# Optimization experiments

Hardware: AMD Instinct MI355X
Metric: run time of the kernel (lower is better)

Reference implementation:

```python
import jax, jax.numpy as jnp
import numpy as np

N_NODES = 160000
N_EDGES = 2560000
N_GRAPHS = 1024
D = 32


def _gcn_layer(x, W, b, row, col, w):
    # PyG GCNConv with add_self_loops=True (loop weight 1) and symmetric norm.
    xw = x @ W                                   # [N, D]
    deg = jax.ops.segment_sum(w, col, num_segments=N_NODES) + 1.0  # self-loop
    dinv = jax.lax.rsqrt(deg)                    # deg >= 1 so finite
    norm = dinv[row] * w * dinv[col]             # [E]
    agg = jax.ops.segment_sum(norm[:, None] * xw[row], col, num_segments=N_NODES)
    agg = agg + xw * (1.0 / deg)[:, None]        # self-loop message: dinv[i]^2 = 1/deg[i]
    return agg + b


def setup_inputs() -> dict:
    key = jax.random.key(0)
    ks = jax.random.split(key, 20)
    s = 0.1
    inp = {
        "x": jax.random.normal(ks[0], (N_NODES, 1), jnp.float32),
        "edge_indices": jax.random.randint(ks[1], (2, N_EDGES), 0, N_NODES),
        "edge_weights": jax.random.uniform(ks[2], (N_EDGES,), jnp.float32),
        "batch": jnp.sort(jax.random.randint(ks[3], (N_NODES,), 0, N_GRAPHS)),
        # pre-MLP (2 layers)
        "W_pre0": s * jax.random.normal(ks[4], (1, D), jnp.float32),
        "b_pre0": jnp.zeros((D,), jnp.float32),
        "W_pre1": s * jax.random.normal(ks[5], (D, D), jnp.float32),
        "b_pre1": jnp.zeros((D,), jnp.float32),
        # 3 GCNConv layers
        "W_g0": s * jax.random.normal(ks[6], (D, D), jnp.float32),
        "b_g0": jnp.zeros((D,), jnp.float32),
        "W_g1": s * jax.random.normal(ks[7], (D, D), jnp.float32),
        "b_g1": jnp.zeros((D,), jnp.float32),
        "W_g2": s * jax.random.normal(ks[8], (D, D), jnp.float32),
        "b_g2": jnp.zeros((D,), jnp.float32),
        # post-MLP (2 layers, last -> 1 + sigmoid)
        "W_post0": s * jax.random.normal(ks[9], (D, D), jnp.float32),
        "b_post0": jnp.zeros((D,), jnp.float32),
        "W_post1": s * jax.random.normal(ks[10], (D, 1), jnp.float32),
        "b_post1": jnp.zeros((1,), jnp.float32),
    }
    return inp


def reference(x, edge_indices, edge_weights, batch,
              W_pre0, b_pre0, W_pre1, b_pre1,
              W_g0, b_g0, W_g1, b_g1, W_g2, b_g2,
              W_post0, b_post0, W_post1, b_post1):
    row, col = edge_indices[0], edge_indices[1]
    # pre-MLP: Linear + ReLU x2
    h = jax.nn.relu(x @ W_pre0 + b_pre0)
    h = jax.nn.relu(h @ W_pre1 + b_pre1)
    h = jax.nn.relu(_gcn_layer(h, W_g0, b_g0, row, col, edge_weights))
    h = jax.nn.relu(_gcn_layer(h, W_g1, b_g1, row, col, edge_weights))
    h = jax.nn.relu(_gcn_layer(h, W_g2, b_g2, row, col, edge_weights))
    # global mean pool over batch ids
    sums = jax.ops.segment_sum(h, batch, num_segments=N_GRAPHS)
    cnts = jax.ops.segment_sum(jnp.ones((N_NODES,), h.dtype), batch, num_segments=N_GRAPHS)
    g = sums / jnp.maximum(cnts, 1.0)[:, None]
    # post-MLP: Linear+ReLU (dropout inactive in eval), then Linear+Sigmoid
    g = jax.nn.relu(g @ W_post0 + b_post0)
    out = jax.nn.sigmoid(g @ W_post1 + b_post1)
    return out
```

## Files before the change

### kernel.cpp

```cpp
#include <hip/hip_runtime.h>
#include <math.h>

#define DIM 32
#define NB 625
#define CAP 5120
#define CHUNK 8192
#define BMAX 7424

typedef float floatx2 __attribute__((ext_vector_type(2)));

__device__ __forceinline__ unsigned pack4_fp8(float a, float b, float c, float d) {
    unsigned v = 0;
    v = __builtin_amdgcn_cvt_pk_fp8_f32(a, b, v, false);
    v = __builtin_amdgcn_cvt_pk_fp8_f32(c, d, v, true);
    return v;
}

__global__ void setup_kernel(const int* __restrict__ batch, int* __restrict__ gptr,
                             int* __restrict__ bcur, int N, int G) {
    int n = blockIdx.x * blockDim.x + threadIdx.x;
    if (n < NB) bcur[n] = n * CAP;
    if (n >= N) return;
    int b = batch[n];
    int bp = (n == 0) ? -1 : batch[n - 1];
    for (int g = bp + 1; g <= b; g++) gptr[g] = n;
    if (n == N - 1) {
        for (int g = b + 1; g <= G; g++) gptr[g] = N;
    }
}

__global__ __launch_bounds__(1024) void passA_kernel(
        const int* __restrict__ row, const int* __restrict__ col,
        const float* __restrict__ w, int* __restrict__ bcur,
        unsigned long long* __restrict__ stage, int E) {
    __shared__ unsigned long long lrec[CHUNK];
    __shared__ int hist[NB];
    __shared__ int excl[NB + 1];
    __shared__ int gbase[NB];
    __shared__ int sc[1024];
    int t = threadIdx.x;
    int base = blockIdx.x * CHUNK;
    int cnt = min(CHUNK, E - base);
    int creg[8];

    for (int j = t; j < NB; j += 1024) hist[j] = 0;
    __syncthreads();

#pragma unroll
    for (int i = 0; i < 8; i++) {
        int e = base + i * 1024 + t;
        creg[i] = (e < E) ? col[e] : -1;
        if (creg[i] >= 0) atomicAdd(&hist[creg[i] >> 8], 1);
    }
    __syncthreads();

    int v = (t < NB) ? hist[t] : 0;
    sc[t] = v;
    __syncthreads();
#pragma unroll
    for (int off = 1; off < 1024; off <<= 1) {
        int u = (t >= off) ? sc[t - off] : 0;
        __syncthreads();
        sc[t] += u;
        __syncthreads();
    }
    if (t < NB) {
        int ex = sc[t] - v;
        excl[t] = ex;
        hist[t] = ex;
        gbase[t] = v ? atomicAdd(&bcur[t], v) : 0;
    }
    if (t == 0) excl[NB] = cnt;
    __syncthreads();

#pragma unroll
    for (int i = 0; i < 8; i++) {
        int e = base + i * 1024 + t;
        int c = creg[i];
        if (c >= 0) {
            unsigned long long rec = ((unsigned long long)(unsigned)row[e] << 40)
                                   | ((unsigned long long)(unsigned)(c & 255) << 32)
                                   | (unsigned long long)__float_as_uint(w[e]);
            int pos = atomicAdd(&hist[c >> 8], 1);
            lrec[pos] = rec;
        }
    }
    __syncthreads();

    for (int i = t; i < cnt; i += 1024) {
        int lo = 0, hi = NB;
        while (hi - lo > 1) {
            int mid = (lo + hi) >> 1;
            if (excl[mid] <= i) lo = mid; else hi = mid;
        }
        int gpos = gbase[lo] + (i - excl[lo]);
        if (gpos < (lo + 1) * CAP) stage[gpos] = lrec[i];
    }
}

__global__ void passB1_kernel(const unsigned long long* __restrict__ stage,
                              const int* __restrict__ bcur,
                              int* __restrict__ cnt, float* __restrict__ dinv) {
    __shared__ int icnt[256];
    __shared__ float fdeg[256];
    int b = blockIdx.x;
    icnt[threadIdx.x] = 0;
    fdeg[threadIdx.x] = 0.0f;
    __syncthreads();
    int s0 = b * CAP;
    int m = min(bcur[b] - s0, CAP);
    for (int i = threadIdx.x; i < m; i += 256) {
        unsigned long long rec = stage[s0 + i];
        int cj = (int)((rec >> 32) & 255);
        float wf = __uint_as_float((unsigned)rec);
        atomicAdd(&icnt[cj], 1);
        atomicAdd(&fdeg[cj], wf);
    }
    __syncthreads();
    int c = b * 256 + threadIdx.x;
    cnt[c] = ((icnt[threadIdx.x] + 8) >> 3) << 3;
    dinv[c] = rsqrtf(fdeg[threadIdx.x] + 1.0f);
}

__global__ void scan_block_kernel(const int* __restrict__ cnt, int* __restrict__ ptr,
                                  int* __restrict__ bsum, int N) {
    __shared__ int s[256];
    int i = blockIdx.x * 256 + threadIdx.x;
    int v = (i < N) ? cnt[i] : 0;
    s[threadIdx.x] = v;
    __syncthreads();
#pragma unroll
    for (int off = 1; off < 256; off <<= 1) {
        int t = (threadIdx.x >= off) ? s[threadIdx.x - off] : 0;
        __syncthreads();
        s[threadIdx.x] += t;
        __syncthreads();
    }
    if (i < N) ptr[i] = s[threadIdx.x] - v;
    if (threadIdx.x == 255) bsum[blockIdx.x] = s[255];
}

__global__ void scan_fin_kernel(int* __restrict__ ptr, const int* __restrict__ bsum,
                                int N) {
    __shared__ int red[256];
    int b = blockIdx.x;
    int t = threadIdx.x;
    int p = 0;
    for (int j = t; j < b; j += 256) p += bsum[j];
    red[t] = p;
    __syncthreads();
#pragma unroll
    for (int off = 128; off > 0; off >>= 1) {
        if (t < off) red[t] += red[t + off];
        __syncthreads();
    }
    int S = red[0];
    int i = b * 256 + t;
    if (i < N) ptr[i] += S;
    if (b == gridDim.x - 1 && t == 0) ptr[N] = S + bsum[b];
}

__global__ void passB2_kernel(const unsigned long long* __restrict__ stage,
                              const int* __restrict__ bcur, const int* __restrict__ ptr,
                              const float* __restrict__ dinv,
                              unsigned* __restrict__ edat) {
    __shared__ unsigned limg[BMAX];
    __shared__ int lcur[256];
    __shared__ int s_pbase, s_pend;
    int b = blockIdx.x;
    int t = threadIdx.x;
    int c = b * 256 + t;
    int p0 = ptr[c];
    if (t == 0) s_pbase = p0;
    if (t == 255) s_pend = ptr[c + 1];
    __syncthreads();
    int pbase = s_pbase;
    int sz = s_pend - pbase;
    lcur[t] = p0 - pbase + 1;
    for (int i = t; i < sz; i += 256) limg[i] = 0;
    __syncthreads();
    float di = dinv[c];
    float d2 = di * di;
    unsigned qs = min((unsigned)(d2 * 16384.0f + 0.5f), 16383u);
    limg[p0 - pbase] = ((unsigned)c << 14) | qs;
    int s0 = b * CAP;
    int m = min(bcur[b] - s0, CAP);
    for (int i = t; i < m; i += 256) {
        unsigned long long rec = stage[s0 + i];
        int r = (int)(rec >> 40);
        int cj = (int)((rec >> 32) & 255);
        float wf = __uint_as_float((unsigned)rec);
        float nm = dinv[r] * wf * dinv[b * 256 + cj];
        unsigned q = (unsigned)(nm * 16384.0f + 0.5f);
        q = min(q, 16383u);
        int pos = atomicAdd(&lcur[cj], 1);
        limg[pos] = ((unsigned)r << 14) | q;
    }
    __syncthreads();
    for (int i = t; i < sz; i += 256) edat[pbase + i] = limg[i];
}

__global__ void pre_kernel(const float* __restrict__ x,
                           const float* __restrict__ W0, const float* __restrict__ b0,
                           const float* __restrict__ W1, const float* __restrict__ b1,
                           const float* __restrict__ Wg,
                           unsigned char* __restrict__ xw8, int N) {
    int n = blockIdx.x * blockDim.x + threadIdx.x;
    if (n >= N) return;
    float xv = x[n];
    float h0[DIM];
#pragma unroll
    for (int k = 0; k < DIM; k++) h0[k] = fmaxf(xv * W0[k] + b0[k], 0.0f);
    float h1[DIM];
#pragma unroll
    for (int d = 0; d < DIM; d++) h1[d] = b1[d];
#pragma unroll
    for (int k = 0; k < DIM; k++) {
        float hk = h0[k];
#pragma unroll
        for (int d = 0; d < DIM; d++) h1[d] += hk * W1[k * DIM + d];
    }
#pragma unroll
    for (int d = 0; d < DIM; d++) h1[d] = fmaxf(h1[d], 0.0f);
    float o[DIM];
#pragma unroll
    for (int d = 0; d < DIM; d++) o[d] = 0.0f;
#pragma unroll
    for (int k = 0; k < DIM; k++) {
        float hk = h1[k];
#pragma unroll
        for (int d = 0; d < DIM; d++) o[d] += hk * Wg[k * DIM + d];
    }
    unsigned u[8];
#pragma unroll
    for (int i = 0; i < 8; i++)
        u[i] = pack4_fp8(o[4 * i], o[4 * i + 1], o[4 * i + 2], o[4 * i + 3]);
    uint4* dst = (uint4*)(xw8 + (size_t)n * 32);
    dst[0] = make_uint4(u[0], u[1], u[2], u[3]);
    dst[1] = make_uint4(u[4], u[5], u[6], u[7]);
}

__device__ __forceinline__ void gather_body(
        const unsigned char* __restrict__ xin, const unsigned* __restrict__ edat,
        int e0, int e1, int slot, int sub, float acc[8]) {
    floatx2 a0 = {0, 0}, a1 = {0, 0}, a2 = {0, 0}, a3 = {0, 0};
    for (int base = e0; base < e1; base += 8) {
        unsigned rec0 = edat[base + slot];
        unsigned rec1 = edat[base + 4 + slot];
        int r0 = (int)(rec0 >> 14);
        int r1 = (int)(rec1 >> 14);
        float nm0 = (float)(rec0 & 16383u) * (1.0f / 16384.0f);
        float nm1 = (float)(rec1 & 16383u) * (1.0f / 16384.0f);
        uint2 u0 = *(const uint2*)(xin + (size_t)r0 * 32 + sub * 8);
        uint2 u1 = *(const uint2*)(xin + (size_t)r1 * 32 + sub * 8);
        floatx2 w0; w0.x = nm0; w0.y = nm0;
        floatx2 w1; w1.x = nm1; w1.y = nm1;
        a0 += w0 * __builtin_amdgcn_cvt_pk_f32_fp8(u0.x, false);
        a1 += w0 * __builtin_amdgcn_cvt_pk_f32_fp8(u0.x, true);
        a2 += w0 * __builtin_amdgcn_cvt_pk_f32_fp8(u0.y, false);
        a3 += w0 * __builtin_amdgcn_cvt_pk_f32_fp8(u0.y, true);
        a0 += w1 * __builtin_amdgcn_cvt_pk_f32_fp8(u1.x, false);
        a1 += w1 * __builtin_amdgcn_cvt_pk_f32_fp8(u1.x, true);
        a2 += w1 * __builtin_amdgcn_cvt_pk_f32_fp8(u1.y, false);
        a3 += w1 * __builtin_amdgcn_cvt_pk_f32_fp8(u1.y, true);
    }
    acc[0] = a0.x; acc[1] = a0.y; acc[2] = a1.x; acc[3] = a1.y;
    acc[4] = a2.x; acc[5] = a2.y; acc[6] = a3.x; acc[7] = a3.y;
#pragma unroll
    for (int s = 8; s >= 4; s >>= 1) {
#pragma unroll
        for (int i = 0; i < 8; i++) acc[i] += __shfl_xor(acc[i], s, 64);
    }
}

__global__ void gm_kernel(const unsigned char* __restrict__ xin,
                          const unsigned* __restrict__ edat,
                          const int* __restrict__ ptr,
                          const float* __restrict__ bgl,
                          const float* __restrict__ Wn,
                          unsigned char* __restrict__ xout, int N) {
    __shared__ float hs[16][33];
    __shared__ float wsm[1024];
    int t = threadIdx.x;
    for (int j = t; j < 1024; j += 256) wsm[j] = Wn[j];
    int wv = (blockIdx.x * blockDim.x + t) >> 6;
    int n0 = wv * 4;
    int lane = t & 63;
    int sg   = lane >> 4;
    int slot = (lane >> 2) & 3;
    int sub  = lane & 3;
    int n = n0 + sg;
    int e0 = ptr[n], e1 = ptr[n + 1];
    float acc[8];
    gather_body(xin, edat, e0, e1, slot, sub, acc);
    if (slot == 0) {
        int ln = (t >> 6) * 4 + sg;
#pragma unroll
        for (int i = 0; i < 8; i++)
            hs[ln][sub * 8 + i] = fmaxf(acc[i] + bgl[sub * 8 + i], 0.0f);
    }
    __syncthreads();
    int ln = t >> 4, dg = t & 15;
    const float* hrow = hs[ln];
    float o0 = 0.0f, o1 = 0.0f;
#pragma unroll
    for (int k = 0; k < DIM; k++) {
        float hk = hrow[k];
        o0 += hk * wsm[k * DIM + dg * 2];
        o1 += hk * wsm[k * DIM + dg * 2 + 1];
    }
    unsigned v = __builtin_amdgcn_cvt_pk_fp8_f32(o0, o1, 0, false);
    int nodeG = blockIdx.x * 16 + ln;
    *(unsigned short*)(xout + (size_t)nodeG * 32 + dg * 2) = (unsigned short)(v & 0xffff);
}

__global__ void gather_kernel(const unsigned char* __restrict__ xw8,
                              const unsigned* __restrict__ edat,
                              const int* __restrict__ ptr,
                              const float* __restrict__ bg,
                              float* __restrict__ agg, int N) {
    int wv = (blockIdx.x * blockDim.x + threadIdx.x) >> 6;
    int n0 = wv * 4;
    if (n0 >= N) return;
    int lane = threadIdx.x & 63;
    int sg   = lane >> 4;
    int slot = (lane >> 2) & 3;
    int sub  = lane & 3;
    int n = n0 + sg;
    int e0 = ptr[n], e1 = ptr[n + 1];
    float acc[8];
    gather_body(xw8, edat, e0, e1, slot, sub, acc);
    if (slot == 0) {
        float4 v0 = make_float4(acc[0] + bg[sub * 8 + 0], acc[1] + bg[sub * 8 + 1],
                                acc[2] + bg[sub * 8 + 2], acc[3] + bg[sub * 8 + 3]);
        float4 v1 = make_float4(acc[4] + bg[sub * 8 + 4], acc[5] + bg[sub * 8 + 5],
                                acc[6] + bg[sub * 8 + 6], acc[7] + bg[sub * 8 + 7]);
        float4* dst = (float4*)(agg + (size_t)n * DIM + sub * 8);
        dst[0] = v0;
        dst[1] = v1;
    }
}

__global__ void pool_post_kernel(const float* __restrict__ agg, const int* __restrict__ gptr,
                                 const float* __restrict__ W0, const float* __restrict__ b0,
                                 const float* __restrict__ W1, const float* __restrict__ b1,
                                 float* __restrict__ out) {
    __shared__ float red[8][DIM];
    __shared__ float gv[DIM];
    __shared__ float pr[DIM];
    int g = blockIdx.x;
    int s0 = gptr[g], s1 = gptr[g + 1];
    int slot = threadIdx.x >> 5, d = threadIdx.x & 31;
    float acc = 0.0f;
    for (int n = s0 + slot; n < s1; n += 8)
        acc += fmaxf(agg[(size_t)n * DIM + d], 0.0f);
    red[slot][d] = acc;
    __syncthreads();
    if (threadIdx.x < DIM) {
        float t = 0.0f;
#pragma unroll
        for (int i = 0; i < 8; i++) t += red[i][threadIdx.x];
        float c = fmaxf((float)(s1 - s0), 1.0f);
        gv[threadIdx.x] = t / c;
    }
    __syncthreads();
    if (threadIdx.x < DIM) {
        int j = threadIdx.x;
        float p = b0[j];
#pragma unroll
        for (int k = 0; k < DIM; k++) p += gv[k] * W0[k * DIM + j];
        pr[j] = fmaxf(p, 0.0f) * W1[j];
    }
    __syncthreads();
    if (threadIdx.x == 0) {
        float a = b1[0];
#pragma unroll
        for (int j = 0; j < DIM; j++) a += pr[j];
        out[g] = 1.0f / (1.0f + expf(-a));
    }
}

extern "C" void kernel_launch(void* const* d_in, const int* in_sizes, int n_in,
                              void* d_out, int out_size, void* d_ws, size_t ws_size,
                              hipStream_t stream) {
    const float* x   = (const float*)d_in[0];
    const int*   ei  = (const int*)d_in[1];
    const float* ew  = (const float*)d_in[2];
    const int*   bat = (const int*)d_in[3];
    const float* Wpre0 = (const float*)d_in[4];
    const float* bpre0 = (const float*)d_in[5];
    const float* Wpre1 = (const float*)d_in[6];
    const float* bpre1 = (const float*)d_in[7];
    const float* Wg[3]  = {(const float*)d_in[8],  (const float*)d_in[10], (const float*)d_in[12]};
    const float* bg[3]  = {(const float*)d_in[9],  (const float*)d_in[11], (const float*)d_in[13]};
    const float* Wpost0 = (const float*)d_in[14];
    const float* bpost0 = (const float*)d_in[15];
    const float* Wpost1 = (const float*)d_in[16];
    const float* bpost1 = (const float*)d_in[17];
    float* out = (float*)d_out;

    const int N = in_sizes[0];
    const int E = in_sizes[2];
    const int G = out_size;
    const int nb = (N + 255) / 256;

    const int* row = ei;
    const int* col = ei + E;

    float* ws = (float*)d_ws;
    size_t nd = (size_t)N * DIM;
    float*          agg   = ws;
    unsigned char*  xw8a  = (unsigned char*)(agg + nd);
    unsigned long long* stage = (unsigned long long*)ws;
    float*          dinv  = ws + nd + nd / 4;
    int*            cnt   = (int*)(dinv + N);
    int*            ptr   = cnt + N;
    int*            bsum  = ptr + (N + 2);
    int*            gptr  = bsum + 626;
    int*            bcur  = gptr + 1026;
    unsigned*       edat  = (unsigned*)(bcur + 626);
    unsigned char*  xw8b  = (unsigned char*)(edat + E + 8 * (size_t)N);

    const int B = 256;

    setup_kernel<<<(N + B - 1) / B, B, 0, stream>>>(bat, gptr, bcur, N, G);
    int nChunksA = (E + CHUNK - 1) / CHUNK;
    passA_kernel<<<nChunksA, 1024, 0, stream>>>(row, col, ew, bcur, stage, E);
    passB1_kernel<<<NB, B, 0, stream>>>(stage, bcur, cnt, dinv);
    scan_block_kernel<<<nb, 256, 0, stream>>>(cnt, ptr, bsum, N);
    scan_fin_kernel<<<nb, 256, 0, stream>>>(ptr, bsum, N);
    passB2_kernel<<<NB, B, 0, stream>>>(stage, bcur, ptr, dinv, edat);

    pre_kernel<<<(N + B - 1) / B, B, 0, stream>>>(
        x, Wpre0, bpre0, Wpre1, bpre1, Wg[0], xw8a, N);

    long long gThreads = (long long)(N / 4) * 64;
    int gBlocks = (int)((gThreads + B - 1) / B);
    int fBlocks = N / 16;

    gm_kernel<<<fBlocks, B, 0, stream>>>(xw8a, edat, ptr, bg[0], Wg[1], xw8b, N);
    gm_kernel<<<fBlocks, B, 0, stream>>>(xw8b, edat, ptr, bg[1], Wg[2], xw8a, N);
    gather_kernel<<<gBlocks, B, 0, stream>>>(xw8a, edat, ptr, bg[2], agg, N);

    pool_post_kernel<<<G, 256, 0, stream>>>(agg, gptr, Wpost0, bpost0, Wpost1, bpost1, out);
}
```

Baseline: 310.1 us.

## Fuse CSR scan into build passes and pool the last layer via atomics

The block-local exclusive scan moves into passB1, and the cross-block offset into passB2, so two separate scan kernels disappear and passB2 writes final CSR pointers itself. The last gather layer now applies bias and ReLU and atomically adds into per-graph sums, with wave-level shuffle reduction when all four nodes belong to one graph. This removes the N×32 float agg round-trip and the pooling kernel's read of it, leaving a small post-MLP kernel. It trades this for float atomics, so the summation order becomes non-deterministic, and for more per-block prefix work in passB2.

```diff
diff --git a/kernel.cpp b/kernel.cpp
--- a/kernel.cpp
+++ b/kernel.cpp
@@ -17,9 +17,11 @@
 }
 
 __global__ void setup_kernel(const int* __restrict__ batch, int* __restrict__ gptr,
-                             int* __restrict__ bcur, int N, int G) {
+                             int* __restrict__ bcur, float* __restrict__ gsum,
+                             int N, int G) {
     int n = blockIdx.x * blockDim.x + threadIdx.x;
     if (n < NB) bcur[n] = n * CAP;
+    if (n < G * DIM) gsum[n] = 0.0f;
     if (n >= N) return;
     int b = batch[n];
     int bp = (n == 0) ? -1 : batch[n - 1];
@@ -100,16 +102,19 @@
 
 __global__ void passB1_kernel(const unsigned long long* __restrict__ stage,
                               const int* __restrict__ bcur,
-                              int* __restrict__ cnt, float* __restrict__ dinv) {
+                              int* __restrict__ ptr, int* __restrict__ bsum,
+                              float* __restrict__ dinv) {
     __shared__ int icnt[256];
     __shared__ float fdeg[256];
+    __shared__ int s[256];
     int b = blockIdx.x;
-    icnt[threadIdx.x] = 0;
-    fdeg[threadIdx.x] = 0.0f;
+    int t = threadIdx.x;
+    icnt[t] = 0;
+    fdeg[t] = 0.0f;
     __syncthreads();
     int s0 = b * CAP;
     int m = min(bcur[b] - s0, CAP);
-    for (int i = threadIdx.x; i < m; i += 256) {
+    for (int i = t; i < m; i += 256) {
         unsigned long long rec = stage[s0 + i];
         int cj = (int)((rec >> 32) & 255);
         float wf = __uint_as_float((unsigned)rec);
@@ -117,34 +122,33 @@
         atomicAdd(&fdeg[cj], wf);
     }
     __syncthreads();
-    int c = b * 256 + threadIdx.x;
-    cnt[c] = ((icnt[threadIdx.x] + 8) >> 3) << 3;
-    dinv[c] = rsqrtf(fdeg[threadIdx.x] + 1.0f);
-}
-
-__global__ void scan_block_kernel(const int* __restrict__ cnt, int* __restrict__ ptr,
-                                  int* __restrict__ bsum, int N) {
-    __shared__ int s[256];
-    int i = blockIdx.x * 256 + threadIdx.x;
-    int v = (i < N) ? cnt[i] : 0;
-    s[threadIdx.x] = v;
+    int c = b * 256 + t;
+    int v = ((icnt[t] + 8) >> 3) << 3;
+    dinv[c] = rsqrtf(fdeg[t] + 1.0f);
+    s[t] = v;
     __syncthreads();
 #pragma unroll
     for (int off = 1; off < 256; off <<= 1) {
-        int t = (threadIdx.x >= off) ? s[threadIdx.x - off] : 0;
+        int u = (t >= off) ? s[t - off] : 0;
         __syncthreads();
-        s[threadIdx.x] += t;
+        s[t] += u;
         __syncthreads();
     }
-    if (i < N) ptr[i] = s[threadIdx.x] - v;
-    if (threadIdx.x == 255) bsum[blockIdx.x] = s[255];
-}
-
-__global__ void scan_fin_kernel(int* __restrict__ ptr, const int* __restrict__ bsum,
-                                int N) {
+    ptr[c] = s[t] - v;
+    if (t == 255) bsum[b] = s[255];
+}
+
+__global__ void passB2_kernel(const unsigned long long* __restrict__ stage,
+                              const int* __restrict__ bcur, int* __restrict__ ptr,
+                              const int* __restrict__ bsum,
+                              const float* __restrict__ dinv,
+                              unsigned* __restrict__ edat, int N) {
+    __shared__ unsigned limg[BMAX];
+    __shared__ int lcur[256];
     __shared__ int red[256];
     int b = blockIdx.x;
     int t = threadIdx.x;
+    int c = b * 256 + t;
     int p = 0;
     for (int j = t; j < b; j += 256) p += bsum[j];
     red[t] = p;
@@ -155,34 +159,15 @@
         __syncthreads();
     }
     int S = red[0];
-    int i = b * 256 + t;
-    if (i < N) ptr[i] += S;
-    if (b == gridDim.x - 1 && t == 0) ptr[N] = S + bsum[b];
-}
-
-__global__ void passB2_kernel(const unsigned long long* __restrict__ stage,
-                              const int* __restrict__ bcur, const int* __restrict__ ptr,
-                              const float* __restrict__ dinv,
-                              unsigned* __restrict__ edat) {
-    __shared__ unsigned limg[BMAX];
-    __shared__ int lcur[256];
-    __shared__ int s_pbase, s_pend;
-    int b = blockIdx.x;
-    int t = threadIdx.x;
-    int c = b * 256 + t;
-    int p0 = ptr[c];
-    if (t == 0) s_pbase = p0;
-    if (t == 255) s_pend = ptr[c + 1];
-    __syncthreads();
-    int pbase = s_pbase;
-    int sz = s_pend - pbase;
-    lcur[t] = p0 - pbase + 1;
-    for (int i = t; i < sz; i += 256) limg[i] = 0;
+    int bs = bsum[b];
+    int pl = ptr[c];
+    lcur[t] = pl + 1;
+    for (int i = t; i < bs; i += 256) limg[i] = 0;
     __syncthreads();
     float di = dinv[c];
     float d2 = di * di;
     unsigned qs = min((unsigned)(d2 * 16384.0f + 0.5f), 16383u);
-    limg[p0 - pbase] = ((unsigned)c << 14) | qs;
+    limg[pl] = ((unsigned)c << 14) | qs;
     int s0 = b * CAP;
     int m = min(bcur[b] - s0, CAP);
     for (int i = t; i < m; i += 256) {
@@ -197,7 +182,9 @@
         limg[pos] = ((unsigned)r << 14) | q;
     }
     __syncthreads();
-    for (int i = t; i < sz; i += 256) edat[pbase + i] = limg[i];
+    for (int i = t; i < bs; i += 256) edat[S + i] = limg[i];
+    ptr[c] = S + pl;
+    if (b == gridDim.x - 1 && t == 255) ptr[N] = S + bs;
 }
 
 __global__ void pre_kernel(const float* __restrict__ x,
@@ -314,11 +301,12 @@
     *(unsigned short*)(xout + (size_t)nodeG * 32 + dg * 2) = (unsigned short)(v & 0xffff);
 }
 
-__global__ void gather_kernel(const unsigned char* __restrict__ xw8,
-                              const unsigned* __restrict__ edat,
-                              const int* __restrict__ ptr,
-                              const float* __restrict__ bg,
-                              float* __restrict__ agg, int N) {
+__global__ void gp_kernel(const unsigned char* __restrict__ xw8,
+                          const unsigned* __restrict__ edat,
+                          const int* __restrict__ ptr,
+                          const int* __restrict__ batch,
+                          const float* __restrict__ bg,
+                          float* __restrict__ gsum, int N) {
     int wv = (blockIdx.x * blockDim.x + threadIdx.x) >> 6;
     int n0 = wv * 4;
     if (n0 >= N) return;
@@ -330,54 +318,50 @@
     int e0 = ptr[n], e1 = ptr[n + 1];
     float acc[8];
     gather_body(xw8, edat, e0, e1, slot, sub, acc);
-    if (slot == 0) {
-        float4 v0 = make_float4(acc[0] + bg[sub * 8 + 0], acc[1] + bg[sub * 8 + 1],
-                                acc[2] + bg[sub * 8 + 2], acc[3] + bg[sub * 8 + 3]);
-        float4 v1 = make_float4(acc[4] + bg[sub * 8 + 4], acc[5] + bg[sub * 8 + 5],
-                                acc[6] + bg[sub * 8 + 6], acc[7] + bg[sub * 8 + 7]);
-        float4* dst = (float4*)(agg + (size_t)n * DIM + sub * 8);
-        dst[0] = v0;
-        dst[1] = v1;
-    }
-}
-
-__global__ void pool_post_kernel(const float* __restrict__ agg, const int* __restrict__ gptr,
-                                 const float* __restrict__ W0, const float* __restrict__ b0,
-                                 const float* __restrict__ W1, const float* __restrict__ b1,
-                                 float* __restrict__ out) {
-    __shared__ float red[8][DIM];
-    __shared__ float gv[DIM];
-    __shared__ float pr[DIM];
-    int g = blockIdx.x;
-    int s0 = gptr[g], s1 = gptr[g + 1];
-    int slot = threadIdx.x >> 5, d = threadIdx.x & 31;
-    float acc = 0.0f;
-    for (int n = s0 + slot; n < s1; n += 8)
-        acc += fmaxf(agg[(size_t)n * DIM + d], 0.0f);
-    red[slot][d] = acc;
-    __syncthreads();
-    if (threadIdx.x < DIM) {
-        float t = 0.0f;
-#pragma unroll
-        for (int i = 0; i < 8; i++) t += red[i][threadIdx.x];
-        float c = fmaxf((float)(s1 - s0), 1.0f);
-        gv[threadIdx.x] = t / c;
-    }
-    __syncthreads();
-    if (threadIdx.x < DIM) {
-        int j = threadIdx.x;
-        float p = b0[j];
-#pragma unroll
-        for (int k = 0; k < DIM; k++) p += gv[k] * W0[k * DIM + j];
-        pr[j] = fmaxf(p, 0.0f) * W1[j];
-    }
-    __syncthreads();
-    if (threadIdx.x == 0) {
-        float a = b1[0];
-#pragma unroll
-        for (int j = 0; j < DIM; j++) a += pr[j];
-        out[g] = 1.0f / (1.0f + expf(-a));
-    }
+    float v[8];
+#pragma unroll
+    for (int i = 0; i < 8; i++) v[i] = fmaxf(acc[i] + bg[sub * 8 + i], 0.0f);
+    int g0 = batch[n0];
+    int g3 = batch[n0 + 3];
+    if (g0 == g3) {
+#pragma unroll
+        for (int i = 0; i < 8; i++) {
+            v[i] += __shfl_xor(v[i], 16, 64);
+            v[i] += __shfl_xor(v[i], 32, 64);
+        }
+        if (lane < 4) {
+#pragma unroll
+            for (int i = 0; i < 8; i++)
+                atomicAdd(&gsum[g0 * DIM + sub * 8 + i], v[i]);
+        }
+    } else {
+        if (slot == 0) {
+            int g = batch[n];
+#pragma unroll
+            for (int i = 0; i < 8; i++)
+                atomicAdd(&gsum[g * DIM + sub * 8 + i], v[i]);
+        }
+    }
+}
+
+__global__ void post_kernel(const float* __restrict__ gsum, const int* __restrict__ gptr,
+                            const float* __restrict__ W0, const float* __restrict__ b0,
+                            const float* __restrict__ W1, const float* __restrict__ b1,
+                            float* __restrict__ out, int G) {
+    __shared__ float gv[8][DIM];
+    int t = threadIdx.x;
+    int li = t & 31, gi = t >> 5;
+    int g = blockIdx.x * 8 + gi;
+    float cnt = fmaxf((float)(gptr[g + 1] - gptr[g]), 1.0f);
+    gv[gi][li] = gsum[g * DIM + li] / cnt;
+    __syncthreads();
+    float p = b0[li];
+#pragma unroll
+    for (int k = 0; k < DIM; k++) p += gv[gi][k] * W0[k * DIM + li];
+    float pj = fmaxf(p, 0.0f) * W1[li];
+#pragma unroll
+    for (int s = 16; s > 0; s >>= 1) pj += __shfl_xor(pj, s, 32);
+    if (li == 0) out[g] = 1.0f / (1.0f + expf(-(pj + b1[0])));
 }
 
 extern "C" void kernel_launch(void* const* d_in, const int* in_sizes, int n_in,
@@ -402,34 +386,30 @@
     const int N = in_sizes[0];
     const int E = in_sizes[2];
     const int G = out_size;
-    const int nb = (N + 255) / 256;
 
     const int* row = ei;
     const int* col = ei + E;
 
     float* ws = (float*)d_ws;
     size_t nd = (size_t)N * DIM;
-    float*          agg   = ws;
-    unsigned char*  xw8a  = (unsigned char*)(agg + nd);
     unsigned long long* stage = (unsigned long long*)ws;
+    unsigned char*  xw8a  = (unsigned char*)(ws + nd);
     float*          dinv  = ws + nd + nd / 4;
-    int*            cnt   = (int*)(dinv + N);
-    int*            ptr   = cnt + N;
+    int*            ptr   = (int*)(dinv + N);
     int*            bsum  = ptr + (N + 2);
     int*            gptr  = bsum + 626;
     int*            bcur  = gptr + 1026;
-    unsigned*       edat  = (unsigned*)(bcur + 626);
+    float*          gsum  = (float*)(bcur + 626);
+    unsigned*       edat  = (unsigned*)(gsum + (size_t)G * DIM);
     unsigned char*  xw8b  = (unsigned char*)(edat + E + 8 * (size_t)N);
 
     const int B = 256;
 
-    setup_kernel<<<(N + B - 1) / B, B, 0, stream>>>(bat, gptr, bcur, N, G);
+    setup_kernel<<<(N + B - 1) / B, B, 0, stream>>>(bat, gptr, bcur, gsum, N, G);
     int nChunksA = (E + CHUNK - 1) / CHUNK;
     passA_kernel<<<nChunksA, 1024, 0, stream>>>(row, col, ew, bcur, stage, E);
-    passB1_kernel<<<NB, B, 0, stream>>>(stage, bcur, cnt, dinv);
-    scan_block_kernel<<<nb, 256, 0, stream>>>(cnt, ptr, bsum, N);
-    scan_fin_kernel<<<nb, 256, 0, stream>>>(ptr, bsum, N);
-    passB2_kernel<<<NB, B, 0, stream>>>(stage, bcur, ptr, dinv, edat);
+    passB1_kernel<<<NB, B, 0, stream>>>(stage, bcur, ptr, bsum, dinv);
+    passB2_kernel<<<NB, B, 0, stream>>>(stage, bcur, ptr, bsum, dinv, edat, N);
 
     pre_kernel<<<(N + B - 1) / B, B, 0, stream>>>(
         x, Wpre0, bpre0, Wpre1, bpre1, Wg[0], xw8a, N);
@@ -440,7 +420,7 @@
 
     gm_kernel<<<fBlocks, B, 0, stream>>>(xw8a, edat, ptr, bg[0], Wg[1], xw8b, N);
     gm_kernel<<<fBlocks, B, 0, stream>>>(xw8b, edat, ptr, bg[1], Wg[2], xw8a, N);
-    gather_kernel<<<gBlocks, B, 0, stream>>>(xw8a, edat, ptr, bg[2], agg, N);
-
-    pool_post_kernel<<<G, 256, 0, stream>>>(agg, gptr, Wpost0, bpost0, Wpost1, bpost1, out);
-}
+    gp_kernel<<<gBlocks, B, 0, stream>>>(xw8a, edat, ptr, bat, bg[2], gsum, N);
+
+    post_kernel<<<G / 8, B, 0, stream>>>(gsum, gptr, Wpost0, bpost0, Wpost1, bpost1, out, G);
+}
```

Result: slower. 376.7 us (+21.5%).
